# Kernel optimization log

Measured on AMD Instinct MI355X. Metric: run time of the kernel, lower is better.

Reference implementation:

```python
import jax, jax.numpy as jnp
import numpy as np

B = 64
BAND = 16384
N_OSC = 32
CH = 64
T_IN = 32
N_NOISE_FRAMES = BAND // 4          # 4096
NOISE_STEP = BAND // N_NOISE_FRAMES  # 4 samples per noise frame
NOISE_COEFFS = NOISE_STEP // 2 + 1   # 3 rfft coefficients
N_UP = int(np.log2(N_NOISE_FRAMES) - np.log2(T_IN))  # 7 doubling blocks
LOWEST_FREQ = 20.0 / 11025.0


def _conv1d(x, w, b, pad):
    # x: (B, Cin, T), w: (Cout, Cin, K)
    out = jax.lax.conv_general_dilated(x, w, (1,), [(pad, pad)],
                                       dimension_numbers=('NCH', 'OIH', 'NCH'))
    return out + b[None, :, None]


def _leaky(x):
    return jnp.where(x > 0, x, 0.2 * x)


def _lin_interp(x, size):
    # torch F.interpolate(mode='linear', align_corners=False) along last axis
    n = x.shape[-1]
    coords = (jnp.arange(size, dtype=jnp.float32) + 0.5) * (n / size) - 0.5
    coords = jnp.clip(coords, 0.0, n - 1.0)
    lo = jnp.floor(coords).astype(jnp.int32)
    hi = jnp.minimum(lo + 1, n - 1)
    frac = (coords - lo.astype(jnp.float32)).astype(x.dtype)
    return x[..., lo] * (1.0 - frac) + x[..., hi] * frac


def setup_inputs() -> dict:
    key = jax.random.key(0)
    ks = jax.random.split(key, 16)
    s = 0.1
    return {
        'x': jax.random.normal(ks[0], (B, T_IN, CH), jnp.float32),
        'noise': jax.random.uniform(ks[1], (B, N_NOISE_FRAMES, NOISE_STEP), jnp.float32, -1.0, 1.0),
        'net_w': jax.random.normal(ks[2], (4, CH, CH, 3), jnp.float32) * s,
        'net_b': jax.random.normal(ks[3], (4, CH), jnp.float32) * s,
        'final_w': jax.random.normal(ks[4], (CH, CH, 3), jnp.float32) * s,
        'final_b': jax.random.normal(ks[5], (CH,), jnp.float32) * s,
        'amp_w': jax.random.normal(ks[6], (N_OSC, CH), jnp.float32) * s,
        'amp_b': jax.random.normal(ks[7], (N_OSC,), jnp.float32) * s,
        'freq_w': jax.random.normal(ks[8], (N_OSC, CH), jnp.float32) * s,
        'freq_b': jax.random.normal(ks[9], (N_OSC,), jnp.float32) * s,
        'nz_init_w': jax.random.normal(ks[10], (CH, CH), jnp.float32) * s,
        'nz_init_b': jax.random.normal(ks[11], (CH,), jnp.float32) * s,
        'nz_up_w': jax.random.normal(ks[12], (N_UP, CH, CH, 3), jnp.float32) * s,
        'nz_up_b': jax.random.normal(ks[13], (N_UP, CH), jnp.float32) * s,
        'nz_final_w': jax.random.normal(ks[14], (NOISE_COEFFS, CH), jnp.float32) * s,
        'nz_final_b': jax.random.normal(ks[15], (NOISE_COEFFS,), jnp.float32) * s,
    }


def reference(x, noise, net_w, net_b, final_w, final_b, amp_w, amp_b, freq_w, freq_b,
              nz_init_w, nz_init_b, nz_up_w, nz_up_b, nz_final_w, nz_final_b):
    z = jnp.transpose(x, (0, 2, 1))  # (B, CH, T_IN)
    for i in range(4):
        z = _leaky(_conv1d(z, net_w[i], net_b[i], 1))
    z = _conv1d(z, final_w, final_b, 1)

    # --- OscillatorBank: sigmoid freq (constrained), abs amp, linear upsample,
    # phase accumulation via cumsum, summed sinusoids ---
    amp = jnp.abs(jnp.einsum('bct,oc->bot', z, amp_w) + amp_b[None, :, None])
    freq = jax.nn.sigmoid(jnp.einsum('bct,oc->bot', z, freq_w) + freq_b[None, :, None])
    freq = LOWEST_FREQ + freq * (1.0 - LOWEST_FREQ)
    amp = _lin_interp(amp, BAND)    # (B, N_OSC, BAND)
    freq = _lin_interp(freq, BAND)  # (B, N_OSC, BAND)
    phase = jnp.cumsum(freq * jnp.pi, axis=-1)
    harm = jnp.sum(amp * jnp.sin(phase), axis=1, keepdims=True)  # (B, 1, BAND)

    # 1x1 conv to rfft coeffs, squared, applied per-frame to uniform noise ---
    y = jnp.einsum('bct,oc->bot', z, nz_init_w) + nz_init_b[None, :, None]
    for i in range(N_UP):
        y = jnp.repeat(y, 2, axis=-1)
        y = _leaky(_conv1d(y, nz_up_w[i], nz_up_b[i], 1))
    coeffs = jnp.einsum('bct,oc->bot', y, nz_final_w) + nz_final_b[None, :, None]
    coeffs = coeffs ** 2                      # squared=True, activation=identity
    coeffs = jnp.transpose(coeffs, (0, 2, 1))  # (B, frames, NOISE_COEFFS)
    spec = jnp.fft.rfft(noise, axis=-1, norm='ortho')   # (B, frames, NOISE_COEFFS)
    filt = spec * coeffs.astype(spec.dtype)
    nz = jnp.fft.irfft(filt, n=NOISE_STEP, axis=-1, norm='ortho')  # (B, frames, step)
    nz = nz.reshape(B, 1, BAND)

    return harm + nz
```

## Files before the change

### kernel.cpp

```cpp
#include <hip/hip_runtime.h>
#include <math.h>

#define LOWEST_FREQ_F 0.00181405895691609977f

typedef short bf16x8 __attribute__((ext_vector_type(8)));
typedef float f32x16 __attribute__((ext_vector_type(16)));

__device__ __forceinline__ float lrelu(float x) { return x > 0.f ? x : 0.2f * x; }
__device__ __forceinline__ float sin_rev(float fr) { return __builtin_amdgcn_sinf(fr); }
__device__ __forceinline__ float bf2f(unsigned short u) {
  union { unsigned int i; float f; } x; x.i = ((unsigned int)u) << 16; return x.f;
}
__device__ __forceinline__ unsigned short f2bf(float f) {
  union { float f; unsigned int i; } x; x.f = f;
  unsigned int r = x.i + 0x7FFFu + ((x.i >> 16) & 1u);
  return (unsigned short)(r >> 16);
}
__device__ __forceinline__ unsigned int pack2(float a, float b) {
  return (unsigned int)f2bf(a) | ((unsigned int)f2bf(b) << 16);
}

__global__ __launch_bounds__(256) void prep_kernel(
    const float* __restrict__ net_w, const float* __restrict__ fin_w,
    const float* __restrict__ amp_w, const float* __restrict__ frq_w,
    const float* __restrict__ nzi_w, const float* __restrict__ nzu_w,
    float* __restrict__ wtF4, float* __restrict__ awfwT,
    float* __restrict__ nzT, short* __restrict__ wfold)
{
  __shared__ __align__(16) float wls[12288];
  const int tid = threadIdx.x;
  const int bx  = blockIdx.x;

  if (bx < 7) {
    const float4* src = (const float4*)(nzu_w + bx * 12288);
    #pragma unroll
    for (int i = 0; i < 12; ++i)
      ((float4*)wls)[tid + i*256] = src[tid + i*256];
    __syncthreads();
    short* dst = wfold + bx * 16384;
    for (int i = 0; i < 64; ++i) {
      int q = i*256 + tid;
      int pd = q >> 12, co = (q >> 6) & 63, ci = q & 63;
      const float* wb = wls + co*192 + ci*3;
      float v;
      if      (pd == 0) v = wb[0];
      else if (pd == 1) v = wb[1] + wb[2];
      else if (pd == 2) v = wb[0] + wb[1];
      else              v = wb[2];
      dst[q] = (short)f2bf(v);
    }
  } else if (bx < 12) {
    int l = bx - 7;
    const float* s0 = (l < 4) ? (net_w + l * 12288) : fin_w;
    const float4* src = (const float4*)s0;
    #pragma unroll
    for (int i = 0; i < 12; ++i)
      ((float4*)wls)[tid + i*256] = src[tid + i*256];
    __syncthreads();
    float4* dst = ((float4*)wtF4) + l * 4096;
    for (int i = 0; i < 16; ++i) {
      int q = i*256 + tid;
      int ci = q >> 6, co = q & 63;
      const float* wb = wls + co*192 + ci*3;
      dst[q] = make_float4(wb[0], wb[1], wb[2], 0.f);
    }
  } else {
    #pragma unroll
    for (int i = 0; i < 2; ++i)
      ((float4*)wls)[tid + i*256] = ((const float4*)amp_w)[tid + i*256];
    #pragma unroll
    for (int i = 0; i < 2; ++i)
      ((float4*)(wls + 2048))[tid + i*256] = ((const float4*)frq_w)[tid + i*256];
    #pragma unroll
    for (int i = 0; i < 4; ++i)
      ((float4*)(wls + 4096))[tid + i*256] = ((const float4*)nzi_w)[tid + i*256];
    __syncthreads();
    for (int i = 0; i < 16; ++i) {
      int q = i*256 + tid;
      int c2 = q >> 7, rem = q & 127, o = rem >> 2, k = rem & 3;
      int c = c2*2 + (k >> 1);
      awfwT[q] = (k & 1) ? wls[2048 + o*64 + c] : wls[o*64 + c];
    }
    for (int i = 0; i < 16; ++i) {
      int q = i*256 + tid;
      int c = q >> 6, o = q & 63;
      nzT[q] = wls[4096 + o*64 + c];
    }
  }
}

template<int TIN>
__device__ __forceinline__ void noise_layer(
    const short* tin, short* tout, const short* __restrict__ wf,
    const float* __restrict__ bias, int tid)
{
  const int L  = tid & 63;
  const int w  = tid >> 6;
  const int mt = w & 1;
  const int ng = w >> 1;

  bf16x8 Af[4][4];
  {
    const short* wb = wf + (mt*32 + (L & 31))*64 + ((L >> 5) << 3);
    #pragma unroll
    for (int pd = 0; pd < 4; ++pd)
      #pragma unroll
      for (int ks = 0; ks < 4; ++ks)
        Af[pd][ks] = *(const bf16x8*)(wb + pd*4096 + ks*16);
  }
  f32x16 binit;
  #pragma unroll
  for (int r = 0; r < 16; ++r)
    binit[r] = bias[mt*32 + (r & 3) + 8*(r >> 2) + 4*(L >> 5)];

  if (tid < 64) { tout[tid] = 0; tout[(2*TIN + 1)*72 + tid] = 0; }

  constexpr int TOT = TIN / 32;
  constexpr int NPG = (TOT + 3) / 4;
  #pragma unroll
  for (int nt = 0; nt < NPG; ++nt) {
    int ntile = ng*NPG + nt;
    if (ntile < TOT) {
      int s = ntile*32 + (L & 31);
      const short* bp = tin + s*72 + ((L >> 5) << 3);
      f32x16 Ce = binit, Co = binit;
      #pragma unroll
      for (int ks = 0; ks < 4; ++ks) {
        bf16x8 Bm = *(const bf16x8*)(bp + ks*16);
        bf16x8 B0 = *(const bf16x8*)(bp + 72 + ks*16);
        bf16x8 Bp = *(const bf16x8*)(bp + 144 + ks*16);
        Ce = __builtin_amdgcn_mfma_f32_32x32x16_bf16(Af[0][ks], Bm, Ce, 0, 0, 0);
        Ce = __builtin_amdgcn_mfma_f32_32x32x16_bf16(Af[1][ks], B0, Ce, 0, 0, 0);
        Co = __builtin_amdgcn_mfma_f32_32x32x16_bf16(Af[2][ks], B0, Co, 0, 0, 0);
        Co = __builtin_amdgcn_mfma_f32_32x32x16_bf16(Af[3][ks], Bp, Co, 0, 0, 0);
      }
      #pragma unroll
      for (int q4 = 0; q4 < 4; ++q4) {
        int co0 = mt*32 + 8*q4 + 4*(L >> 5);
        uint2 ve, vo;
        ve.x = pack2(lrelu(Ce[4*q4+0]), lrelu(Ce[4*q4+1]));
        ve.y = pack2(lrelu(Ce[4*q4+2]), lrelu(Ce[4*q4+3]));
        vo.x = pack2(lrelu(Co[4*q4+0]), lrelu(Co[4*q4+1]));
        vo.y = pack2(lrelu(Co[4*q4+2]), lrelu(Co[4*q4+3]));
        *(uint2*)&tout[(2*s + 1)*72 + co0] = ve;
        *(uint2*)&tout[(2*s + 2)*72 + co0] = vo;
      }
    }
  }
  __syncthreads();
}

template<int NT, int ROFF, bool TOGLOBAL>
__device__ __forceinline__ void up_stage(
    const short* bin, short* bout, unsigned short* gout,
    const short* __restrict__ wf, const float* __restrict__ bias, int tid)
{
  const int L  = tid & 63;
  const int w  = tid >> 6;
  const int mt = w & 1;
  const int pg = w >> 1;

  bf16x8 Af[4][4];
  {
    const short* wb = wf + (mt*32 + (L & 31))*64 + ((L >> 5) << 3);
    #pragma unroll
    for (int pd = 0; pd < 4; ++pd)
      #pragma unroll
      for (int ks = 0; ks < 4; ++ks)
        Af[pd][ks] = *(const bf16x8*)(wb + pd*4096 + ks*16);
  }
  f32x16 binit;
  #pragma unroll
  for (int r = 0; r < 16; ++r)
    binit[r] = bias[mt*32 + (r & 3) + 8*(r >> 2) + 4*(L >> 5)];

  for (int n = pg; n < NT; n += 2) {
    int sl = n*32 + (L & 31);
    const short* bp = bin + (sl + ROFF)*72 + ((L >> 5) << 3);
    f32x16 Ce = binit, Co = binit;
    #pragma unroll
    for (int ks = 0; ks < 4; ++ks) {
      bf16x8 Bm = *(const bf16x8*)(bp + ks*16);
      bf16x8 B0 = *(const bf16x8*)(bp + 72 + ks*16);
      bf16x8 Bp = *(const bf16x8*)(bp + 144 + ks*16);
      Ce = __builtin_amdgcn_mfma_f32_32x32x16_bf16(Af[0][ks], Bm, Ce, 0, 0, 0);
      Ce = __builtin_amdgcn_mfma_f32_32x32x16_bf16(Af[1][ks], B0, Ce, 0, 0, 0);
      Co = __builtin_amdgcn_mfma_f32_32x32x16_bf16(Af[2][ks], B0, Co, 0, 0, 0);
      Co = __builtin_amdgcn_mfma_f32_32x32x16_bf16(Af[3][ks], Bp, Co, 0, 0, 0);
    }
    #pragma unroll
    for (int q4 = 0; q4 < 4; ++q4) {
      int co0 = mt*32 + 8*q4 + 4*(L >> 5);
      uint2 ve, vo;
      ve.x = pack2(lrelu(Ce[4*q4+0]), lrelu(Ce[4*q4+1]));
      ve.y = pack2(lrelu(Ce[4*q4+2]), lrelu(Ce[4*q4+3]));
      vo.x = pack2(lrelu(Co[4*q4+0]), lrelu(Co[4*q4+1]));
      vo.y = pack2(lrelu(Co[4*q4+2]), lrelu(Co[4*q4+3]));
      if (TOGLOBAL) {
        *(uint2*)(gout + (size_t)(2*sl)*64 + co0)     = ve;
        *(uint2*)(gout + (size_t)(2*sl + 1)*64 + co0) = vo;
      } else {
        *(uint2*)&bout[(2*sl)*72 + co0]     = ve;
        *(uint2*)&bout[(2*sl + 1)*72 + co0] = vo;
      }
    }
  }
}

__global__ __launch_bounds__(256) void up345(
    const unsigned short* __restrict__ y3, unsigned short* __restrict__ y6,
    const short* __restrict__ wfold, const float* __restrict__ nzu_b)
{
  __shared__ __align__(16) short s3[66*72];
  __shared__ __align__(16) short s4[128*72];
  __shared__ __align__(16) short s5[192*72];

  const int b   = blockIdx.y;
  const int bx  = blockIdx.x;
  const int tid = threadIdx.x;

  const unsigned short* inb = y3 + (size_t)b * 256 * 64;
  for (int c = tid; c < 66*8; c += 256) {
    int row = c >> 3, pos = (c & 7) << 3;
    int g = 32*bx - 2 + row;
    bf16x8 v = {0,0,0,0,0,0,0,0};
    if (g >= 0 && g < 256) v = *(const bf16x8*)(inb + (size_t)g*64 + pos);
    *(bf16x8*)&s3[row*72 + pos] = v;
  }
  __syncthreads();

  up_stage<2,0,false>(s3, s4, nullptr, wfold + 3*16384, nzu_b + 3*64, tid);
  __syncthreads();
  if (bx == 0) {
    if (tid < 128) s4[(tid >> 6)*72 + (tid & 63)] = 0;
  } else if (bx == 7) {
    for (int i = tid; i < 62*64; i += 256) {
      int r = 66 + (i >> 6);
      s4[r*72 + (i & 63)] = 0;
    }
  }
  __syncthreads();

  up_stage<3,0,false>(s4, s5, nullptr, wfold + 4*16384, nzu_b + 4*64, tid);
  __syncthreads();
  if (bx == 0) {
    if (tid < 128) s5[(tid >> 6)*72 + (tid & 63)] = 0;
  } else if (bx == 7) {
    for (int i = tid; i < 62*64; i += 256) {
      int r = 130 + (i >> 6);
      s5[r*72 + (i & 63)] = 0;
    }
  }
  __syncthreads();

  unsigned short* outb = y6 + ((size_t)b*2048 + 256*bx) * 64;
  up_stage<4,1,true>(s5, nullptr, outb, wfold + 5*16384, nzu_b + 5*64, tid);
}

__global__ __launch_bounds__(512) void z_front(
    const float* __restrict__ x, const float* __restrict__ wtF4,
    const float* __restrict__ net_b, const float* __restrict__ fin_b,
    const float* __restrict__ awfwT, const float* __restrict__ amp_b,
    const float* __restrict__ frq_b,
    const float* __restrict__ nzT, const float* __restrict__ nzi_b,
    const short* __restrict__ wfold, const float* __restrict__ nzu_b,
    unsigned short* __restrict__ y3, float* __restrict__ amp_o,
    float* __restrict__ frq_o, float* __restrict__ ph_o)
{
  __shared__ __align__(16) char arena[86976];
  short* tileB = (short*)arena;
  short* tileA = (short*)(arena + 37152);
  float* za    = (float*)(arena + 55872);
  float* zb    = (float*)(arena + 65088);
  float* zt    = (float*)(arena + 74304);
  float* fl    = (float*)(arena + 82752);

  const int b   = blockIdx.x;
  const int tid = threadIdx.x;
  const int co  = tid & 63;
  const int wv  = tid >> 6;

  for (int idx = tid; idx < 2048; idx += 512) {
    int t = idx >> 6, c = idx & 63;
    za[c*36 + t + 1] = x[b*2048 + idx];
  }
  if (tid < 64) {
    za[tid*36] = 0.f; za[tid*36 + 33] = 0.f;
    zb[tid*36] = 0.f; zb[tid*36 + 33] = 0.f;
  }
  __syncthreads();

  float* pa = za;
  float* pb = zb;
  for (int l = 0; l < 5; ++l) {
    {
      const int t0 = wv << 2;
      float bv = (l < 4) ? net_b[l*64 + co] : fin_b[co];
      float acc[4];
      #pragma unroll
      for (int j = 0; j < 4; ++j) acc[j] = bv;

      const float4* wp = ((const float4*)wtF4) + l*4096 + co;
      float4 wCur[8], wNxt[8];
      #pragma unroll
      for (int k = 0; k < 8; ++k) wCur[k] = wp[k*64];

      for (int cc = 0; cc < 8; ++cc) {
        if (cc < 7) {
          #pragma unroll
          for (int k = 0; k < 8; ++k) wNxt[k] = wp[((cc+1)*8 + k)*64];
        }
        #pragma unroll
        for (int k = 0; k < 8; ++k) {
          const int ci = cc*8 + k;
          const float* rowp = pa + ci*36 + t0;
          float4 zA = *(const float4*)(rowp);
          float2 zB = *(const float2*)(rowp + 4);
          float rr[6] = {zA.x, zA.y, zA.z, zA.w, zB.x, zB.y};
          float4 wgt = wCur[k];
          #pragma unroll
          for (int j = 0; j < 4; ++j) {
            acc[j] = fmaf(wgt.x, rr[j],   acc[j]);
            acc[j] = fmaf(wgt.y, rr[j+1], acc[j]);
            acc[j] = fmaf(wgt.z, rr[j+2], acc[j]);
          }
        }
        if (cc < 7) {
          #pragma unroll
          for (int k = 0; k < 8; ++k) wCur[k] = wNxt[k];
        }
      }

      if (l < 4) {
        #pragma unroll
        for (int j = 0; j < 4; ++j)
          pb[co*36 + t0 + j + 1] = lrelu(acc[j]);
      } else {
        #pragma unroll
        for (int j = 0; j < 4; ++j) {
          int t = t0 + j;
          pb[co*36 + t] = acc[j];
          zt[t*66 + co] = acc[j];
        }
      }
    }
    __syncthreads();
    float* tp = pa; pa = pb; pb = tp;
  }
  const float* zf = pa;

  {
    const int q = wv;
    float bv0 = nzi_b[co];
    float acc[4];
    #pragma unroll
    for (int j = 0; j < 4; ++j) acc[j] = bv0;
    #pragma unroll 8
    for (int c = 0; c < 64; ++c) {
      float4 zv = *(const float4*)(zf + c*36 + (q << 2));
      float wvv = nzT[c*64 + co];
      acc[0] = fmaf(wvv, zv.x, acc[0]);
      acc[1] = fmaf(wvv, zv.y, acc[1]);
      acc[2] = fmaf(wvv, zv.z, acc[2]);
      acc[3] = fmaf(wvv, zv.w, acc[3]);
    }
    #pragma unroll
    for (int j = 0; j < 4; ++j)
      tileA[((q << 2) + j + 1)*72 + co] = (short)f2bf(acc[j]);
  }
  if (tid < 64) { tileA[tid] = 0; tileA[33*72 + tid] = 0; }

  #pragma unroll
  for (int tt = 0; tt < 2; ++tt) {
    int task = tid + 512*tt;
    int o = task & 31, t = task >> 5;
    float aa = amp_b[o], ff = frq_b[o];
    #pragma unroll 8
    for (int c2 = 0; c2 < 32; ++c2) {
      float4 w4 = ((const float4*)awfwT)[c2*32 + o];
      float2 zv = *(const float2*)(zt + t*66 + c2*2);
      aa = fmaf(w4.x, zv.x, aa); ff = fmaf(w4.y, zv.x, ff);
      aa = fmaf(w4.z, zv.y, aa); ff = fmaf(w4.w, zv.y, ff);
    }
    aa = fabsf(aa);
    float sg = 1.f / (1.f + expf(-ff));
    float fq = LOWEST_FREQ_F + sg * (1.f - LOWEST_FREQ_F);
    amp_o[b*1024 + o*32 + t] = aa;
    frq_o[b*1024 + o*32 + t] = fq;
    fl[o*33 + t] = fq;
  }
  __syncthreads();

  if (wv == 7 && (tid & 63) < 32) {
    const int o = tid & 31;
    double P = 256.0 * (double)fl[o*33];
    double hd = P * 0.5;
    ph_o[b*1024 + o*32] = (float)(hd - floor(hd));
    for (int i = 1; i < 32; ++i) {
      P += 256.0 * ((double)fl[o*33 + i - 1] + (double)fl[o*33 + i]);
      hd = P * 0.5;
      ph_o[b*1024 + o*32 + i] = (float)(hd - floor(hd));
    }
  }

  noise_layer<32> (tileA, tileB, wfold + 0*16384, nzu_b + 0*64, tid);
  noise_layer<64> (tileB, tileA, wfold + 1*16384, nzu_b + 1*64, tid);
  noise_layer<128>(tileA, tileB, wfold + 2*16384, nzu_b + 2*64, tid);

  unsigned short* yb = y3 + (size_t)b * 16384;
  for (int c = tid; c < 2048; c += 512) {
    int row = c >> 3, pos = (c & 7) << 3;
    *(bf16x8*)(yb + c*8) = *(const bf16x8*)&tileB[(row + 1)*72 + pos];
  }
}

__global__ __launch_bounds__(256) void final_fused(
    const unsigned short* __restrict__ in,
    const short* __restrict__ wf, const float* __restrict__ bias,
    const float* __restrict__ nzf_w, const float* __restrict__ nzf_b,
    const float* __restrict__ noise,
    const float* __restrict__ amp, const float* __restrict__ frq,
    const float* __restrict__ ph, float* __restrict__ out)
{
  constexpr int STILE = 128, Tin = 2048, ROWS = STILE + 2, G = STILE / 64;
  __shared__ __align__(16) short lB[ROWS * 72];
  __shared__ __align__(16) short yT[256 * 72];
  __shared__ float al[1024], fqv[1024], pl[1024];
  __shared__ float wl[192];

  const int b   = blockIdx.y;
  const int s0  = blockIdx.x * STILE;
  const int tid = threadIdx.x;
  const int L   = tid & 63;
  const int w   = tid >> 6;
  const int mt  = w & 1;
  const int ng  = w >> 1;

  for (int i = tid; i < 1024; i += 256) {
    al[i]  = amp[b*1024 + i];
    fqv[i] = frq[b*1024 + i];
    pl[i]  = ph[b*1024 + i];
  }
  if (tid < 192) { int o = tid >> 6, c = tid & 63; wl[c*3 + o] = nzf_w[tid]; }

  bf16x8 Af[4][4];
  {
    const short* wb = wf + (mt*32 + (L & 31))*64 + ((L >> 5) << 3);
    #pragma unroll
    for (int pd = 0; pd < 4; ++pd)
      #pragma unroll
      for (int ks = 0; ks < 4; ++ks)
        Af[pd][ks] = *(const bf16x8*)(wb + pd*4096 + ks*16);
  }

  const unsigned short* inb = in + (size_t)b * Tin * 64;
  for (int c = tid; c < ROWS*8; c += 256) {
    int row = c >> 3, pos = (c & 7) << 3;
    int g = s0 - 1 + row;
    bf16x8 v = {0,0,0,0,0,0,0,0};
    if (g >= 0 && g < Tin) v = *(const bf16x8*)(inb + (size_t)g*64 + pos);
    *(bf16x8*)&lB[row*72 + pos] = v;
  }

  f32x16 binit;
  #pragma unroll
  for (int r = 0; r < 16; ++r)
    binit[r] = bias[mt*32 + (r & 3) + 8*(r >> 2) + 4*(L >> 5)];

  __syncthreads();

  #pragma unroll
  for (int nt = 0; nt < G; ++nt) {
    int s_loc = ng*(32*G) + nt*32 + (L & 31);
    const short* bp = lB + s_loc*72 + ((L >> 5) << 3);
    f32x16 Ce = binit, Co = binit;
    #pragma unroll
    for (int ks = 0; ks < 4; ++ks) {
      bf16x8 Bm = *(const bf16x8*)(bp + ks*16);
      bf16x8 B0 = *(const bf16x8*)(bp + 72 + ks*16);
      bf16x8 Bp = *(const bf16x8*)(bp + 144 + ks*16);
      Ce = __builtin_amdgcn_mfma_f32_32x32x16_bf16(Af[0][ks], Bm, Ce, 0, 0, 0);
      Ce = __builtin_amdgcn_mfma_f32_32x32x16_bf16(Af[1][ks], B0, Ce, 0, 0, 0);
      Co = __builtin_amdgcn_mfma_f32_32x32x16_bf16(Af[2][ks], B0, Co, 0, 0, 0);
      Co = __builtin_amdgcn_mfma_f32_32x32x16_bf16(Af[3][ks], Bp, Co, 0, 0, 0);
    }
    #pragma unroll
    for (int q4 = 0; q4 < 4; ++q4) {
      int co0 = mt*32 + 8*q4 + 4*(L >> 5);
      uint2 ve, vo;
      ve.x = pack2(lrelu(Ce[4*q4+0]), lrelu(Ce[4*q4+1]));
      ve.y = pack2(lrelu(Ce[4*q4+2]), lrelu(Ce[4*q4+3]));
      vo.x = pack2(lrelu(Co[4*q4+0]), lrelu(Co[4*q4+1]));
      vo.y = pack2(lrelu(Co[4*q4+2]), lrelu(Co[4*q4+3]));
      *(uint2*)&yT[(2*s_loc)*72 + co0]     = ve;
      *(uint2*)&yT[(2*s_loc + 1)*72 + co0] = vo;
    }
  }
  __syncthreads();

  {
    const short* yr = &yT[tid * 72];
    float c0 = nzf_b[0], c1 = nzf_b[1], c2 = nzf_b[2];
    #pragma unroll
    for (int c8 = 0; c8 < 8; ++c8) {
      bf16x8 v = *(const bf16x8*)(yr + c8*8);
      #pragma unroll
      for (int j = 0; j < 8; ++j) {
        float yv = bf2f((unsigned short)v[j]);
        int c = c8*8 + j;
        c0 = fmaf(wl[c*3+0], yv, c0);
        c1 = fmaf(wl[c*3+1], yv, c1);
        c2 = fmaf(wl[c*3+2], yv, c2);
      }
    }
    c0 *= c0; c1 *= c1; c2 *= c2;

    const int fb = 2*s0 + tid;
    const float4 n = *(const float4*)(noise + ((size_t)b*4096 + fb)*4);
    float F0  = c0 * (n.x + n.y + n.z + n.w) * 0.5f;
    float F1r = c1 * (n.x - n.z) * 0.5f;
    float F1i = -(c1 * (n.y - n.w) * 0.5f);
    float F2  = c2 * (n.x - n.y + n.z - n.w) * 0.5f;
    float r0 = 0.5f * (F0 + 2.f*F1r + F2);
    float r1 = 0.5f * (F0 - 2.f*F1i - F2);
    float r2 = 0.5f * (F0 - 2.f*F1r + F2);
    float r3 = 0.5f * (F0 + 2.f*F1i - F2);

    const int t0 = fb * 4;
    float s0a = 0.f, s1a = 0.f, s2a = 0.f, s3a = 0.f;
    if (t0 < 256) {
      const float tp = (float)(t0 + 1) * 0.5f;
      #pragma unroll 4
      for (int o = 0; o < 32; ++o) {
        float f0 = fqv[o*32], am = al[o*32];
        float hf = 0.5f * f0;
        float v0 = tp * f0, v1 = v0 + hf, v2 = v1 + hf, v3 = v2 + hf;
        s0a += am * sin_rev(v0 - floorf(v0));
        s1a += am * sin_rev(v1 - floorf(v1));
        s2a += am * sin_rev(v2 - floorf(v2));
        s3a += am * sin_rev(v3 - floorf(v3));
      }
    } else if (t0 >= 16128) {
      const float tp = (float)(t0 - 16127) * 0.5f;
      #pragma unroll 4
      for (int o = 0; o < 32; ++o) {
        float f0 = fqv[o*32 + 31], am = al[o*32 + 31], p = pl[o*32 + 31];
        float hf = 0.5f * f0;
        float v0 = p + tp * f0, v1 = v0 + hf, v2 = v1 + hf, v3 = v2 + hf;
        s0a += am * sin_rev(v0 - floorf(v0));
        s1a += am * sin_rev(v1 - floorf(v1));
        s2a += am * sin_rev(v2 - floorf(v2));
        s3a += am * sin_rev(v3 - floorf(v3));
      }
    } else {
      const int i  = (t0 - 256) >> 9;
      const int m0 = (t0 - 256) & 511;
      float mm[4], fa[4], mq[4];
      #pragma unroll
      for (int js = 0; js < 4; ++js) {
        float mmv = (float)(m0 + 1 + js);
        mm[js] = mmv;
        fa[js] = ((float)(m0 + js) + 0.5f) * (1.f/512.f);
        mq[js] = mmv * mmv * (1.f/1024.f);
      }
      #pragma unroll 4
      for (int o = 0; o < 32; ++o) {
        float f0 = fqv[o*32 + i], f1 = fqv[o*32 + i + 1];
        float a0 = al[o*32 + i],  a1 = al[o*32 + i + 1];
        float p  = pl[o*32 + i];
        float df = f1 - f0, da = a1 - a0;
        #pragma unroll
        for (int js = 0; js < 4; ++js) {
          float av   = fmaf(da, fa[js], a0);
          float part = fmaf(df, mq[js], mm[js] * f0);
          float v    = fmaf(part, 0.5f, p);
          float fr   = v - floorf(v);
          float sv   = av * sin_rev(fr);
          if      (js == 0) s0a += sv;
          else if (js == 1) s1a += sv;
          else if (js == 2) s2a += sv;
          else              s3a += sv;
        }
      }
    }
    float4 res = make_float4(s0a + r0, s1a + r1, s2a + r2, s3a + r3);
    *(float4*)(out + ((size_t)b*4096 + fb)*4) = res;
  }
}

extern "C" void kernel_launch(void* const* d_in, const int* in_sizes, int n_in,
                              void* d_out, int out_size, void* d_ws, size_t ws_size,
                              hipStream_t stream) {
  (void)in_sizes; (void)n_in; (void)out_size; (void)ws_size;
  const float* x     = (const float*)d_in[0];
  const float* noise = (const float*)d_in[1];
  const float* net_w = (const float*)d_in[2];
  const float* net_b = (const float*)d_in[3];
  const float* fin_w = (const float*)d_in[4];
  const float* fin_b = (const float*)d_in[5];
  const float* amp_w = (const float*)d_in[6];
  const float* amp_b = (const float*)d_in[7];
  const float* frq_w = (const float*)d_in[8];
  const float* frq_b = (const float*)d_in[9];
  const float* nzi_w = (const float*)d_in[10];
  const float* nzi_b = (const float*)d_in[11];
  const float* nzu_w = (const float*)d_in[12];
  const float* nzu_b = (const float*)d_in[13];
  const float* nzf_w = (const float*)d_in[14];
  const float* nzf_b = (const float*)d_in[15];
  float* out = (float*)d_out;

  short* y3    = (short*)d_ws;
  short* y6    = y3 + (size_t)64*256*64;
  short* wfold = y6 + (size_t)64*2048*64;
  float* wtF4  = (float*)(wfold + 7*16384);
  float* awfwT = wtF4 + 81920;
  float* nzT   = awfwT + 4096;
  float* ampv  = nzT + 4096;
  float* frqv  = ampv + 65536;
  float* phv   = frqv + 65536;

  prep_kernel<<<dim3(13), dim3(256), 0, stream>>>(
      net_w, fin_w, amp_w, frq_w, nzi_w, nzu_w, wtF4, awfwT, nzT, wfold);

  z_front<<<dim3(64), dim3(512), 0, stream>>>(
      x, wtF4, net_b, fin_b, awfwT, amp_b, frq_b, nzT, nzi_b,
      wfold, nzu_b, (unsigned short*)y3, ampv, frqv, phv);

  up345<<<dim3(8, 64), dim3(256), 0, stream>>>(
      (unsigned short*)y3, (unsigned short*)y6, wfold, nzu_b);

  final_fused<<<dim3(16, 64), dim3(256), 0, stream>>>(
      (unsigned short*)y6, wfold + 6*16384, nzu_b + 6*64,
      nzf_w, nzf_b, noise, ampv, frqv, phv, out);
}
```

Before: 211.9 us.

## Move first three noise upsample layers from z_front into tiled up345 kernel

The first three noise upsampling conv layers move out of the single-block-per-batch z_front kernel into the 8-way tiled up345 kernel. Each tile recomputes a small halo region from the 32-frame input, with predicated writes that keep only valid rows. This lets z_front use far less shared memory, so two blocks can fit per CU, and it removes the 256-row intermediate round trip through global memory. The z_front conv loop is also changed to double-buffer both weight and activation loads. The cost is redundant halo computation, a full shared-memory zeroing pass, and more stages inside up345.

```diff
diff --git a/kernel.cpp b/kernel.cpp
--- a/kernel.cpp
+++ b/kernel.cpp
@@ -89,71 +89,11 @@
   }
 }
 
-template<int TIN>
-__device__ __forceinline__ void noise_layer(
-    const short* tin, short* tout, const short* __restrict__ wf,
-    const float* __restrict__ bias, int tid)
-{
-  const int L  = tid & 63;
-  const int w  = tid >> 6;
-  const int mt = w & 1;
-  const int ng = w >> 1;
-
-  bf16x8 Af[4][4];
-  {
-    const short* wb = wf + (mt*32 + (L & 31))*64 + ((L >> 5) << 3);
-    #pragma unroll
-    for (int pd = 0; pd < 4; ++pd)
-      #pragma unroll
-      for (int ks = 0; ks < 4; ++ks)
-        Af[pd][ks] = *(const bf16x8*)(wb + pd*4096 + ks*16);
-  }
-  f32x16 binit;
-  #pragma unroll
-  for (int r = 0; r < 16; ++r)
-    binit[r] = bias[mt*32 + (r & 3) + 8*(r >> 2) + 4*(L >> 5)];
-
-  if (tid < 64) { tout[tid] = 0; tout[(2*TIN + 1)*72 + tid] = 0; }
-
-  constexpr int TOT = TIN / 32;
-  constexpr int NPG = (TOT + 3) / 4;
-  #pragma unroll
-  for (int nt = 0; nt < NPG; ++nt) {
-    int ntile = ng*NPG + nt;
-    if (ntile < TOT) {
-      int s = ntile*32 + (L & 31);
-      const short* bp = tin + s*72 + ((L >> 5) << 3);
-      f32x16 Ce = binit, Co = binit;
-      #pragma unroll
-      for (int ks = 0; ks < 4; ++ks) {
-        bf16x8 Bm = *(const bf16x8*)(bp + ks*16);
-        bf16x8 B0 = *(const bf16x8*)(bp + 72 + ks*16);
-        bf16x8 Bp = *(const bf16x8*)(bp + 144 + ks*16);
-        Ce = __builtin_amdgcn_mfma_f32_32x32x16_bf16(Af[0][ks], Bm, Ce, 0, 0, 0);
-        Ce = __builtin_amdgcn_mfma_f32_32x32x16_bf16(Af[1][ks], B0, Ce, 0, 0, 0);
-        Co = __builtin_amdgcn_mfma_f32_32x32x16_bf16(Af[2][ks], B0, Co, 0, 0, 0);
-        Co = __builtin_amdgcn_mfma_f32_32x32x16_bf16(Af[3][ks], Bp, Co, 0, 0, 0);
-      }
-      #pragma unroll
-      for (int q4 = 0; q4 < 4; ++q4) {
-        int co0 = mt*32 + 8*q4 + 4*(L >> 5);
-        uint2 ve, vo;
-        ve.x = pack2(lrelu(Ce[4*q4+0]), lrelu(Ce[4*q4+1]));
-        ve.y = pack2(lrelu(Ce[4*q4+2]), lrelu(Ce[4*q4+3]));
-        vo.x = pack2(lrelu(Co[4*q4+0]), lrelu(Co[4*q4+1]));
-        vo.y = pack2(lrelu(Co[4*q4+2]), lrelu(Co[4*q4+3]));
-        *(uint2*)&tout[(2*s + 1)*72 + co0] = ve;
-        *(uint2*)&tout[(2*s + 2)*72 + co0] = vo;
-      }
-    }
-  }
-  __syncthreads();
-}
-
-template<int NT, int ROFF, bool TOGLOBAL>
-__device__ __forceinline__ void up_stage(
+template<int NT, bool TOGLOBAL>
+__device__ __forceinline__ void up_stage2(
     const short* bin, short* bout, unsigned short* gout,
-    const short* __restrict__ wf, const float* __restrict__ bias, int tid)
+    const short* __restrict__ wf, const float* __restrict__ bias, int tid,
+    int roff, int pairbase, int smin, int smax)
 {
   const int L  = tid & 63;
   const int w  = tid >> 6;
@@ -176,7 +116,7 @@
 
   for (int n = pg; n < NT; n += 2) {
     int sl = n*32 + (L & 31);
-    const short* bp = bin + (sl + ROFF)*72 + ((L >> 5) << 3);
+    const short* bp = bin + (sl + roff)*72 + ((L >> 5) << 3);
     f32x16 Ce = binit, Co = binit;
     #pragma unroll
     for (int ks = 0; ks < 4; ++ks) {
@@ -188,6 +128,9 @@
       Co = __builtin_amdgcn_mfma_f32_32x32x16_bf16(Af[2][ks], B0, Co, 0, 0, 0);
       Co = __builtin_amdgcn_mfma_f32_32x32x16_bf16(Af[3][ks], Bp, Co, 0, 0, 0);
     }
+    const int s0 = 2*(sl + pairbase);
+    const bool we = (s0 >= smin)     && (s0 < smax);
+    const bool wo = (s0 + 1 >= smin) && (s0 + 1 < smax);
     #pragma unroll
     for (int q4 = 0; q4 < 4; ++q4) {
       int co0 = mt*32 + 8*q4 + 4*(L >> 5);
@@ -197,83 +140,111 @@
       vo.x = pack2(lrelu(Co[4*q4+0]), lrelu(Co[4*q4+1]));
       vo.y = pack2(lrelu(Co[4*q4+2]), lrelu(Co[4*q4+3]));
       if (TOGLOBAL) {
-        *(uint2*)(gout + (size_t)(2*sl)*64 + co0)     = ve;
-        *(uint2*)(gout + (size_t)(2*sl + 1)*64 + co0) = vo;
+        if (we) *(uint2*)(gout + (size_t)(2*sl)*64 + co0)     = ve;
+        if (wo) *(uint2*)(gout + (size_t)(2*sl + 1)*64 + co0) = vo;
       } else {
-        *(uint2*)&bout[(2*sl)*72 + co0]     = ve;
-        *(uint2*)&bout[(2*sl + 1)*72 + co0] = vo;
+        if (we) *(uint2*)&bout[(2*sl)*72 + co0]     = ve;
+        if (wo) *(uint2*)&bout[(2*sl + 1)*72 + co0] = vo;
       }
     }
   }
 }
 
 __global__ __launch_bounds__(256) void up345(
-    const unsigned short* __restrict__ y3, unsigned short* __restrict__ y6,
+    const unsigned short* __restrict__ y0g, unsigned short* __restrict__ y6,
     const short* __restrict__ wfold, const float* __restrict__ nzu_b)
 {
-  __shared__ __align__(16) short s3[66*72];
-  __shared__ __align__(16) short s4[128*72];
-  __shared__ __align__(16) short s5[192*72];
+  __shared__ __align__(16) short arena[521 * 72];
+  short* y0b = arena;
+  short* y1b = arena + 34*72;
+  short* y2b = arena + 69*72;
+  short* s3  = arena + 135*72;
+  short* s4  = arena + 201*72;
+  short* s5  = arena + 329*72;
 
   const int b   = blockIdx.y;
   const int bx  = blockIdx.x;
   const int tid = threadIdx.x;
 
-  const unsigned short* inb = y3 + (size_t)b * 256 * 64;
-  for (int c = tid; c < 66*8; c += 256) {
+  for (int i = tid; i < 4689; i += 256) ((uint4*)arena)[i] = make_uint4(0,0,0,0);
+  __syncthreads();
+
+  const unsigned short* inb = y0g + (size_t)b * 32 * 64;
+  for (int c = tid; c < 34*8; c += 256) {
     int row = c >> 3, pos = (c & 7) << 3;
-    int g = 32*bx - 2 + row;
-    bf16x8 v = {0,0,0,0,0,0,0,0};
-    if (g >= 0 && g < 256) v = *(const bf16x8*)(inb + (size_t)g*64 + pos);
-    *(bf16x8*)&s3[row*72 + pos] = v;
-  }
-  __syncthreads();
-
-  up_stage<2,0,false>(s3, s4, nullptr, wfold + 3*16384, nzu_b + 3*64, tid);
-  __syncthreads();
-  if (bx == 0) {
-    if (tid < 128) s4[(tid >> 6)*72 + (tid & 63)] = 0;
-  } else if (bx == 7) {
-    for (int i = tid; i < 62*64; i += 256) {
-      int r = 66 + (i >> 6);
-      s4[r*72 + (i & 63)] = 0;
-    }
-  }
-  __syncthreads();
-
-  up_stage<3,0,false>(s4, s5, nullptr, wfold + 4*16384, nzu_b + 4*64, tid);
-  __syncthreads();
-  if (bx == 0) {
-    if (tid < 128) s5[(tid >> 6)*72 + (tid & 63)] = 0;
-  } else if (bx == 7) {
-    for (int i = tid; i < 62*64; i += 256) {
-      int r = 130 + (i >> 6);
-      s5[r*72 + (i & 63)] = 0;
-    }
-  }
+    int g = 4*bx - 2 + row;
+    if (g >= 0 && g < 32)
+      *(bf16x8*)&y0b[row*72 + pos] = *(const bf16x8*)(inb + (size_t)g*64 + pos);
+  }
+  __syncthreads();
+
+  int lo, hi;
+  lo = 8*bx - 2;   hi = 8*bx + 18;
+  up_stage2<1,false>(y0b, y1b, nullptr, wfold + 0*16384, nzu_b + 0*64, tid,
+                     0, 4*bx - 1, lo < 0 ? 0 : lo, hi > 64 ? 64 : hi);
+  __syncthreads();
+  lo = 16*bx - 2;  hi = 16*bx + 33;
+  up_stage2<1,false>(y1b, y2b, nullptr, wfold + 1*16384, nzu_b + 1*64, tid,
+                     0, 8*bx - 1, lo < 0 ? 0 : lo, hi > 128 ? 128 : hi);
+  __syncthreads();
+  lo = 32*bx - 2;  hi = 32*bx + 64;
+  up_stage2<2,false>(y2b, s3, nullptr, wfold + 2*16384, nzu_b + 2*64, tid,
+                     0, 16*bx - 1, lo < 0 ? 0 : lo, hi > 256 ? 256 : hi);
+  __syncthreads();
+  lo = 64*bx - 2;  hi = 64*bx + 126;
+  up_stage2<2,false>(s3, s4, nullptr, wfold + 3*16384, nzu_b + 3*64, tid,
+                     0, 32*bx - 1, lo < 0 ? 0 : lo, hi > 512 ? 512 : hi);
+  __syncthreads();
+  lo = 128*bx - 2; hi = 128*bx + 190;
+  up_stage2<3,false>(s4, s5, nullptr, wfold + 4*16384, nzu_b + 4*64, tid,
+                     0, 64*bx - 1, lo < 0 ? 0 : lo, hi > 1024 ? 1024 : hi);
   __syncthreads();
 
   unsigned short* outb = y6 + ((size_t)b*2048 + 256*bx) * 64;
-  up_stage<4,1,true>(s5, nullptr, outb, wfold + 5*16384, nzu_b + 5*64, tid);
-}
-
-__global__ __launch_bounds__(512) void z_front(
+  up_stage2<4,true>(s5, nullptr, outb, wfold + 5*16384, nzu_b + 5*64, tid,
+                    1, 128*bx, 0, 1 << 30);
+}
+
+__device__ __forceinline__ void load_w8(float4* W, const float4* wp, int cc) {
+  #pragma unroll
+  for (int k = 0; k < 8; ++k) W[k] = wp[(cc*8 + k)*64];
+}
+__device__ __forceinline__ void load_z8(float* Z, const float* pa, int cc, int t0) {
+  #pragma unroll
+  for (int k = 0; k < 8; ++k) {
+    const float* r = pa + (cc*8 + k)*36 + t0;
+    float4 a = *(const float4*)r;
+    float2 b2 = *(const float2*)(r + 4);
+    Z[k*6+0] = a.x; Z[k*6+1] = a.y; Z[k*6+2] = a.z;
+    Z[k*6+3] = a.w; Z[k*6+4] = b2.x; Z[k*6+5] = b2.y;
+  }
+}
+__device__ __forceinline__ void fma8(float* acc, const float4* W, const float* Z) {
+  #pragma unroll
+  for (int k = 0; k < 8; ++k) {
+    #pragma unroll
+    for (int j = 0; j < 4; ++j) {
+      acc[j] = fmaf(W[k].x, Z[k*6+j],   acc[j]);
+      acc[j] = fmaf(W[k].y, Z[k*6+j+1], acc[j]);
+      acc[j] = fmaf(W[k].z, Z[k*6+j+2], acc[j]);
+    }
+  }
+}
+
+__global__ __launch_bounds__(512, 2) void z_front(
     const float* __restrict__ x, const float* __restrict__ wtF4,
     const float* __restrict__ net_b, const float* __restrict__ fin_b,
     const float* __restrict__ awfwT, const float* __restrict__ amp_b,
     const float* __restrict__ frq_b,
     const float* __restrict__ nzT, const float* __restrict__ nzi_b,
-    const short* __restrict__ wfold, const float* __restrict__ nzu_b,
-    unsigned short* __restrict__ y3, float* __restrict__ amp_o,
+    unsigned short* __restrict__ y0g, float* __restrict__ amp_o,
     float* __restrict__ frq_o, float* __restrict__ ph_o)
 {
-  __shared__ __align__(16) char arena[86976];
-  short* tileB = (short*)arena;
-  short* tileA = (short*)(arena + 37152);
-  float* za    = (float*)(arena + 55872);
-  float* zb    = (float*)(arena + 65088);
-  float* zt    = (float*)(arena + 74304);
-  float* fl    = (float*)(arena + 82752);
+  __shared__ __align__(16) char arena[31104];
+  float* za = (float*)arena;
+  float* zb = (float*)(arena + 9216);
+  float* zt = (float*)(arena + 18432);
+  float* fl = (float*)(arena + 26880);
 
   const int b   = blockIdx.x;
   const int tid = threadIdx.x;
@@ -301,33 +272,19 @@
       for (int j = 0; j < 4; ++j) acc[j] = bv;
 
       const float4* wp = ((const float4*)wtF4) + l*4096 + co;
-      float4 wCur[8], wNxt[8];
+      float4 wA[8], wB[8];
+      float  zA[48], zB[48];
+      load_w8(wA, wp, 0);
+      load_z8(zA, pa, 0, t0);
+
       #pragma unroll
-      for (int k = 0; k < 8; ++k) wCur[k] = wp[k*64];
-
       for (int cc = 0; cc < 8; ++cc) {
-        if (cc < 7) {
-          #pragma unroll
-          for (int k = 0; k < 8; ++k) wNxt[k] = wp[((cc+1)*8 + k)*64];
-        }
-        #pragma unroll
-        for (int k = 0; k < 8; ++k) {
-          const int ci = cc*8 + k;
-          const float* rowp = pa + ci*36 + t0;
-          float4 zA = *(const float4*)(rowp);
-          float2 zB = *(const float2*)(rowp + 4);
-          float rr[6] = {zA.x, zA.y, zA.z, zA.w, zB.x, zB.y};
-          float4 wgt = wCur[k];
-          #pragma unroll
-          for (int j = 0; j < 4; ++j) {
-            acc[j] = fmaf(wgt.x, rr[j],   acc[j]);
-            acc[j] = fmaf(wgt.y, rr[j+1], acc[j]);
-            acc[j] = fmaf(wgt.z, rr[j+2], acc[j]);
-          }
-        }
-        if (cc < 7) {
-          #pragma unroll
-          for (int k = 0; k < 8; ++k) wCur[k] = wNxt[k];
+        if (cc & 1) {
+          if (cc < 7) { load_w8(wA, wp, cc + 1); load_z8(zA, pa, cc + 1, t0); }
+          fma8(acc, wB, zB);
+        } else {
+          if (cc < 7) { load_w8(wB, wp, cc + 1); load_z8(zB, pa, cc + 1, t0); }
+          fma8(acc, wA, zA);
         }
       }
 
@@ -364,11 +321,11 @@
       acc[2] = fmaf(wvv, zv.z, acc[2]);
       acc[3] = fmaf(wvv, zv.w, acc[3]);
     }
+    unsigned short* yb = y0g + (size_t)b * 2048;
     #pragma unroll
     for (int j = 0; j < 4; ++j)
-      tileA[((q << 2) + j + 1)*72 + co] = (short)f2bf(acc[j]);
-  }
-  if (tid < 64) { tileA[tid] = 0; tileA[33*72 + tid] = 0; }
+      yb[((q << 2) + j)*64 + co] = f2bf(acc[j]);
+  }
 
   #pragma unroll
   for (int tt = 0; tt < 2; ++tt) {
@@ -401,16 +358,6 @@
       hd = P * 0.5;
       ph_o[b*1024 + o*32 + i] = (float)(hd - floor(hd));
     }
-  }
-
-  noise_layer<32> (tileA, tileB, wfold + 0*16384, nzu_b + 0*64, tid);
-  noise_layer<64> (tileB, tileA, wfold + 1*16384, nzu_b + 1*64, tid);
-  noise_layer<128>(tileA, tileB, wfold + 2*16384, nzu_b + 2*64, tid);
-
-  unsigned short* yb = y3 + (size_t)b * 16384;
-  for (int c = tid; c < 2048; c += 512) {
-    int row = c >> 3, pos = (c & 7) << 3;
-    *(bf16x8*)(yb + c*8) = *(const bf16x8*)&tileB[(row + 1)*72 + pos];
   }
 }
 
@@ -610,8 +557,8 @@
   const float* nzf_b = (const float*)d_in[15];
   float* out = (float*)d_out;
 
-  short* y3    = (short*)d_ws;
-  short* y6    = y3 + (size_t)64*256*64;
+  short* y0    = (short*)d_ws;
+  short* y6    = y0 + (size_t)64*32*64;
   short* wfold = y6 + (size_t)64*2048*64;
   float* wtF4  = (float*)(wfold + 7*16384);
   float* awfwT = wtF4 + 81920;
@@ -625,10 +572,10 @@
 
   z_front<<<dim3(64), dim3(512), 0, stream>>>(
       x, wtF4, net_b, fin_b, awfwT, amp_b, frq_b, nzT, nzi_b,
-      wfold, nzu_b, (unsigned short*)y3, ampv, frqv, phv);
+      (unsigned short*)y0, ampv, frqv, phv);
 
   up345<<<dim3(8, 64), dim3(256), 0, stream>>>(
-      (unsigned short*)y3, (unsigned short*)y6, wfold, nzu_b);
+      (unsigned short*)y0, (unsigned short*)y6, wfold, nzu_b);
 
   final_fused<<<dim3(16, 64), dim3(256), 0, stream>>>(
       (unsigned short*)y6, wfold + 6*16384, nzu_b + 6*64,
```

Result: faster. 207.7 us (-2.0%).
